# Performance work log

Hardware: AMD Instinct MI355X
Metric: run time of the kernel (lower is better)

Reference implementation:

```python
import jax, jax.numpy as jnp
import numpy as np

B, N, C, D, UP, KNN, MULT, PH = 4, 2048, 256, 64, 4, 20, 4, 64
EPS = 1e-5


def conv1d(x, w, b):
    # x: (B, Cin, N), w: (Cout, Cin)
    return jnp.einsum('oc,bcn->bon', w, x) + b[None, :, None]


def conv2d(x, w, b):
    # x: (B, Cin, N, K), 1x1 conv
    return jnp.einsum('oc,bcnk->bonk', w, x) + b[None, :, None, None]


def bn2d(x, g, bt, rm, rv):
    # eval-mode BatchNorm2d with running stats
    inv = jax.lax.rsqrt(rv + EPS)
    return g[None, :, None, None] * (x - rm[None, :, None, None]) * inv[None, :, None, None] + bt[None, :, None, None]


def group(f, idx):
    # f: (B, C, N), idx: (B, N, K) -> (B, C, N, K)
    return jax.vmap(lambda fb, ib: fb[:, ib])(f, idx)


def setup_inputs() -> dict:
    k0 = jax.random.key(0)
    ks = iter(jax.random.split(k0, 48))
    nx = lambda: next(ks)
    rn = lambda shape, s=0.05: jax.random.normal(nx(), shape, dtype=jnp.float32) * s
    z = lambda n: jnp.zeros((n,), jnp.float32)
    o = lambda n: jnp.ones((n,), jnp.float32)
    inp = {
        'pos': jax.random.normal(nx(), (B, 3, N), dtype=jnp.float32),
        'key': jax.random.normal(nx(), (B, C, N), dtype=jnp.float32),
        'query': jax.random.normal(nx(), (B, C, N), dtype=jnp.float32),
        # MLP_Res (mlp_v): in_dim=2C, hidden=C, out=C
        'wv1': rn((C, 2 * C)), 'bv1': z(C),
        'wv2': rn((C, C)), 'bv2': z(C),
        'wvs': rn((C, 2 * C)), 'bvs': z(C),
        # key/query/value projections to dim D
        'wk': rn((D, C)), 'bk': z(D),
        'wq': rn((D, C)), 'bq': z(D),
        'wval': rn((D, C)), 'bval': z(D),
        # pos_mlp: Conv2d(3,PH) -> BN -> ReLU -> Conv2d(PH,D)
        'pw1': rn((PH, 3)), 'pb1': z(PH), 'pg': o(PH), 'pbt': z(PH), 'prm': z(PH), 'prv': o(PH),
        'pw2': rn((D, PH)), 'pb2': z(D),
        # attn_mlp: Conv2d(D, D*MULT) -> BN -> ReLU -> ConvTranspose2d(D*MULT, D, (UP,1), (UP,1))
        'aw1': rn((D * MULT, D)), 'ab1': z(D * MULT), 'ag': o(D * MULT), 'abt': z(D * MULT), 'arm': z(D * MULT), 'arv': o(D * MULT),
        'ctw': rn((D * MULT, D, UP)), 'ctb': z(D),
        # conv_end: Conv1d(D, C)
        'we': rn((C, D)), 'be': z(C),
    }
    return inp


def reference(pos, key, query, wv1, bv1, wv2, bv2, wvs, bvs, wk, bk, wq, bq, wval, bval,
              pw1, pb1, pg, pbt, prm, prv, pw2, pb2,
              aw1, ab1, ag, abt, arm, arv, ctw, ctb, we, be):
    # mlp_v (MLP_Res) on concat([key, query])
    x = jnp.concatenate([key, query], axis=1)  # (B, 2C, N)
    value = conv1d(jax.nn.relu(conv1d(x, wv1, bv1)), wv2, bv2) + conv1d(x, wvs, bvs)  # (B, C, N)
    identity = value

    k_f = conv1d(key, wk, bk)      # (B, D, N)
    q_f = conv1d(query, wq, bq)    # (B, D, N)
    v_f = conv1d(value, wval, bval)

    # KNN (include_self=True): smallest-KNN indices of pairwise sq distance
    p = jnp.transpose(pos, (0, 2, 1))  # (B, N, 3)
    sq = jnp.sum(p * p, axis=-1)
    dist = sq[:, :, None] + sq[:, None, :] - 2.0 * jnp.einsum('bnc,bmc->bnm', p, p)
    idx = jax.lax.top_k(-dist, KNN)[1]  # (B, N, KNN)

    k_g = group(k_f, idx)                              # (B, D, N, KNN)
    qk_rel = q_f[:, :, :, None] - k_g
    pos_rel = pos[:, :, :, None] - group(pos, idx)     # (B, 3, N, KNN)

    h = jax.nn.relu(bn2d(conv2d(pos_rel, pw1, pb1), pg, pbt, prm, prv))
    pos_emb = conv2d(h, pw2, pb2)                      # (B, D, N, KNN)

    a = jax.nn.relu(bn2d(conv2d(qk_rel + pos_emb, aw1, ab1), ag, abt, arm, arv))  # (B, D*MULT, N, KNN)
    # ConvTranspose2d with kernel=(UP,1), stride=(UP,1): non-overlapping, out[b,o,n*UP+r,k]
    ct = jnp.einsum('bcnk,cor->bornk', a, ctw)         # (B, D, UP, N, KNN)
    Bv = a.shape[0]
    ct = jnp.transpose(ct, (0, 1, 3, 2, 4)).reshape(Bv, D, N * UP, KNN) + ctb[None, :, None, None]
    attn = jax.nn.softmax(ct, axis=-1)                 # softmax over neighbors

    v_g = group(v_f, idx) + pos_emb                    # (B, D, N, KNN)
    v_up = jnp.repeat(v_g, UP, axis=2)                 # nearest Upsample (UP,1)
    agg = jnp.sum(attn * v_up, axis=-1)                # (B, D, N*UP)
    y = conv1d(agg, we, be)                            # (B, C, N*UP)
    return y + jnp.repeat(identity, UP, axis=2)
```

## Files before the change

### kernel.cpp

```cpp
#include <hip/hip_runtime.h>
#include <hip/hip_bf16.h>

#define Bq 4
#define Nq 2048
#define Cq 256
#define Dq 64
#define UPq 4
#define KNNq 20
#define PHq 64
#define DMq 256
#define PTS 16

typedef __attribute__((ext_vector_type(8))) short short8;
typedef __attribute__((ext_vector_type(4))) short short4v;
typedef __attribute__((ext_vector_type(4))) float f32x4;
typedef __hip_bfloat16 bf16;

__device__ __forceinline__ unsigned short f2b(float x){
  bf16 h = __float2bfloat16(x);
  return *reinterpret_cast<unsigned short*>(&h);
}
__device__ __forceinline__ float b2f(short s){
  return __bfloat162float(*reinterpret_cast<bf16*>(&s));
}

__device__ __forceinline__ void swz(const float* __restrict__ src,
                                    short* __restrict__ dst,
                                    int M, int K, int g, bool transp)
{
  int j = g & 7, lane = (g >> 3) & 63, rest = g >> 9;
  int KS = K >> 5;
  int ks = rest % KS, mt = rest / KS;
  int m = mt*16 + (lane & 15);
  int k = ks*32 + ((lane >> 4) << 3) + j;
  float v = transp ? src[k*M + m] : src[m*K + k];
  dst[g] = (short)f2b(v);
}

__device__ __forceinline__ void swz_s(const float* __restrict__ src,
                                      short* __restrict__ dst,
                                      int M, int K, int g,
                                      const float* __restrict__ gam,
                                      const float* __restrict__ var)
{
  int j = g & 7, lane = (g >> 3) & 63, rest = g >> 9;
  int KS = K >> 5;
  int ks = rest % KS, mt = rest / KS;
  int m = mt*16 + (lane & 15);
  int k = ks*32 + ((lane >> 4) << 3) + j;
  float sc = gam[m] * rsqrtf(var[m] + 1e-5f);
  dst[g] = (short)f2b(src[m*K + k] * sc);
}

__global__ __launch_bounds__(256) void k_prep(
    const float* __restrict__ aw1, const float* __restrict__ ctw,
    const float* __restrict__ wv1, const float* __restrict__ wvs,
    const float* __restrict__ wv2, const float* __restrict__ wk,
    const float* __restrict__ wq,  const float* __restrict__ wval,
    const float* __restrict__ pw2, const float* __restrict__ we,
    short* __restrict__ aw1b, short* __restrict__ ctwT,
    short* __restrict__ wv1b, short* __restrict__ wvsb,
    short* __restrict__ wv2b, short* __restrict__ wkb,
    short* __restrict__ wqb,  short* __restrict__ wvalb,
    short* __restrict__ pw2b, short* __restrict__ web,
    const float* __restrict__ ag, const float* __restrict__ arv)
{
  const int t = threadIdx.x, bidx = blockIdx.x;
  if (bidx < 512){
    swz(wv1, wv1b, 256, 512, bidx*256 + t, false);
  } else if (bidx < 1024){
    swz(wvs, wvsb, 256, 512, (bidx-512)*256 + t, false);
  } else if (bidx < 1280){
    swz(wv2, wv2b, 256, 256, (bidx-1024)*256 + t, false);
  } else if (bidx < 1344){
    swz(wk, wkb, 64, 256, (bidx-1280)*256 + t, false);
  } else if (bidx < 1408){
    swz(wq, wqb, 64, 256, (bidx-1344)*256 + t, false);
  } else if (bidx < 1472){
    swz(wval, wvalb, 64, 256, (bidx-1408)*256 + t, false);
  } else if (bidx < 1488){
    swz(pw2, pw2b, 64, 64, (bidx-1472)*256 + t, false);
  } else if (bidx < 1552){
    swz_s(aw1, aw1b, 256, 64, (bidx-1488)*256 + t, ag, arv);
  } else if (bidx < 1616){
    swz(we, web, 256, 64, (bidx-1552)*256 + t, false);
  } else {
    swz(ctw, ctwT, 256, 256, (bidx-1616)*256 + t, true);
  }
}

__global__ __launch_bounds__(256, 4) void k_vk(
    const float* __restrict__ key, const float* __restrict__ query,
    const short* __restrict__ wv1b, const short* __restrict__ wvsb,
    const short* __restrict__ wv2b, const short* __restrict__ wkb,
    const short* __restrict__ wqb,  const short* __restrict__ wvalb,
    const float* __restrict__ bv1, const float* __restrict__ bv2,
    const float* __restrict__ bvs, const float* __restrict__ bk,
    const float* __restrict__ bq,  const float* __restrict__ bval,
    float* __restrict__ valueT, short* __restrict__ kfT,
    short* __restrict__ qfT,    short* __restrict__ vfT,
    const float* __restrict__ pos, int* __restrict__ idxT)
{
  const int t = threadIdx.x;
  const int lane = t & 63, w = t >> 6;
  const int vb = blockIdx.x / 5, rem = blockIdx.x % 5;

  if (rem == 4){
    __shared__ __align__(16) short Xb[16*520];
    __shared__ __align__(16) short hidB[16*264];
    __shared__ __align__(16) short valB[16*264];
    const int b = vb >> 7;
    const int n0 = (vb & 127) * PTS;
    const int quad = lane >> 4, l15 = lane & 15;

    {
      const int c4 = t >> 2, pq = t & 3;
      #pragma unroll
      for (int pass=0; pass<4; pass++){
        int c = pass*64 + c4;
        float4 kv = *reinterpret_cast<const float4*>(key   + ((size_t)(b*Cq+c))*Nq + n0 + pq*4);
        float4 qv = *reinterpret_cast<const float4*>(query + ((size_t)(b*Cq+c))*Nq + n0 + pq*4);
        const float* kf_ = (const float*)&kv;
        const float* qf_ = (const float*)&qv;
        #pragma unroll
        for (int i=0;i<4;i++){
          Xb[(pq*4+i)*520 + c]       = (short)f2b(kf_[i]);
          Xb[(pq*4+i)*520 + 256 + c] = (short)f2b(qf_[i]);
        }
      }
    }
    __syncthreads();

    f32x4 acc1[4], accS[4];
    #pragma unroll
    for (int jm=0;jm<4;jm++){ acc1[jm]=(f32x4)0.f; accS[jm]=(f32x4)0.f; }

    #pragma unroll
    for (int ks=0;ks<16;ks++){
      const int kcol = ks*32 + quad*8;
      short8 xb = *reinterpret_cast<const short8*>(&Xb[l15*520 + kcol]);
      #pragma unroll
      for (int jm=0;jm<4;jm++){
        int mt = w*4 + jm;
        short8 a1 = *reinterpret_cast<const short8*>(wv1b + ((mt*16+ks)*64 + lane)*8);
        short8 as = *reinterpret_cast<const short8*>(wvsb + ((mt*16+ks)*64 + lane)*8);
        acc1[jm] = __builtin_amdgcn_mfma_f32_16x16x32_bf16(a1, xb, acc1[jm], 0,0,0);
        accS[jm] = __builtin_amdgcn_mfma_f32_16x16x32_bf16(as, xb, accS[jm], 0,0,0);
      }
    }
    #pragma unroll
    for (int jm=0;jm<4;jm++){
      #pragma unroll
      for (int r=0;r<4;r++){
        int h = (w*4+jm)*16 + quad*4 + r;
        hidB[l15*264 + h] = (short)f2b(fmaxf(acc1[jm][r] + bv1[h], 0.f));
      }
    }
    __syncthreads();

    #pragma unroll
    for (int ks=0;ks<8;ks++){
      const int kcol = ks*32 + quad*8;
      short8 hb = *reinterpret_cast<const short8*>(&hidB[l15*264 + kcol]);
      #pragma unroll
      for (int jm=0;jm<4;jm++){
        int mt = w*4 + jm;
        short8 a = *reinterpret_cast<const short8*>(wv2b + ((mt*8+ks)*64 + lane)*8);
        accS[jm] = __builtin_amdgcn_mfma_f32_16x16x32_bf16(a, hb, accS[jm], 0,0,0);
      }
    }
    #pragma unroll
    for (int jm=0;jm<4;jm++){
      const int cb = (w*4+jm)*16 + quad*4;
      float4 v4;
      #pragma unroll
      for (int r=0;r<4;r++){
        int c = cb + r;
        float v = accS[jm][r] + bv2[c] + bvs[c];
        ((float*)&v4)[r] = v;
        valB[l15*264 + c] = (short)f2b(v);
      }
      *reinterpret_cast<float4*>(valueT + ((size_t)(b*Nq + n0 + l15))*Cq + cb) = v4;
    }
    __syncthreads();

    {
      f32x4 pk4=(f32x4)0.f, pq4=(f32x4)0.f, pv4=(f32x4)0.f;
      #pragma unroll
      for (int ks=0;ks<8;ks++){
        const int kcol = ks*32 + quad*8;
        short8 xk = *reinterpret_cast<const short8*>(&Xb[l15*520 + kcol]);
        short8 xq = *reinterpret_cast<const short8*>(&Xb[l15*520 + 256 + kcol]);
        short8 xv = *reinterpret_cast<const short8*>(&valB[l15*264 + kcol]);
        short8 ak = *reinterpret_cast<const short8*>(wkb  + ((w*8+ks)*64 + lane)*8);
        short8 aq = *reinterpret_cast<const short8*>(wqb  + ((w*8+ks)*64 + lane)*8);
        short8 av = *reinterpret_cast<const short8*>(wvalb+ ((w*8+ks)*64 + lane)*8);
        pk4 = __builtin_amdgcn_mfma_f32_16x16x32_bf16(ak, xk, pk4, 0,0,0);
        pq4 = __builtin_amdgcn_mfma_f32_16x16x32_bf16(aq, xq, pq4, 0,0,0);
        pv4 = __builtin_amdgcn_mfma_f32_16x16x32_bf16(av, xv, pv4, 0,0,0);
      }
      short4v ok, oq, ov;
      #pragma unroll
      for (int r=0;r<4;r++){
        int o = w*16 + quad*4 + r;
        ok[r] = (short)f2b(pk4[r] + bk[o]);
        oq[r] = (short)f2b(pq4[r] + bq[o]);
        ov[r] = (short)f2b(pv4[r] + bval[o]);
      }
      int n = n0 + l15;
      size_t base = ((size_t)(b*Nq+n))*Dq + w*16 + quad*4;
      *reinterpret_cast<short4v*>(kfT + base) = ok;
      *reinterpret_cast<short4v*>(qfT + base) = oq;
      *reinterpret_cast<short4v*>(vfT + base) = ov;
    }
  } else {
    const int kb = vb*4 + rem;
    const int pid = kb*4 + w;
    const int b = pid >> 11;
    const int n = pid & (Nq-1);
    const float* px = pos + (size_t)(b*3+0)*Nq;
    const float* py = pos + (size_t)(b*3+1)*Nq;
    const float* pz = pos + (size_t)(b*3+2)*Nq;
    const float xn=px[n], yn=py[n], zn=pz[n];
    const float sqn = __fadd_rn(__fadd_rn(__fmul_rn(xn,xn),__fmul_rn(yn,yn)),__fmul_rn(zn,zn));

    double kd[32];
    #pragma unroll
    for (int i=0;i<32;i++){
      int j = i*64 + lane;
      float x=px[j], y=py[j], z=pz[j];
      float sqj = __fadd_rn(__fadd_rn(__fmul_rn(x,x),__fmul_rn(y,y)),__fmul_rn(z,z));
      float dot = __fadd_rn(__fadd_rn(__fmul_rn(xn,x),__fmul_rn(yn,y)),__fmul_rn(zn,z));
      float d   = __fsub_rn(__fadd_rn(sqn,sqj), __fmul_rn(2.0f,dot));
      unsigned u = __float_as_uint(d);
      u ^= ((unsigned)((int)u >> 31)) | 0x80000000u;
      kd[i] = (double)u * 2048.0 + (double)j;
    }

    const double BIG = 9.0e15;
    double b0=BIG, b1=BIG, b2=BIG, b3=BIG;
    #pragma unroll
    for (int i=0;i<32;i++){
      double x = kd[i];
      double M0 = fmax(b0, x);  b0 = fmin(b0, x);
      double M1 = fmax(b1, M0); b1 = fmin(b1, M0);
      double M2 = fmax(b2, M1); b2 = fmin(b2, M1);
      b3 = fmin(b3, M2);
    }

    double lane_last = -1.0;
    int cnt = 0;
    for (int s=0;s<KNNq;s++){
      double m = b0;
      #pragma unroll
      for (int off=1; off<64; off<<=1)
        m = fmin(m, __shfl_xor(m, off));
      if (lane == 0){
        unsigned long long kk = (unsigned long long)m;
        idxT[(size_t)pid*KNNq + s] = (int)(kk & 2047ull);
      }
      if (b0 == m){
        lane_last = b0;
        b0 = b1; b1 = b2; b2 = b3; b3 = BIG;
        cnt++;
      }
      if (__any(cnt >= 4)){
        if (cnt >= 4){
          b0 = BIG; b1 = BIG; b2 = BIG; b3 = BIG;
          #pragma unroll
          for (int i=0;i<32;i++){
            double x = (kd[i] > lane_last) ? kd[i] : BIG;
            double M0 = fmax(b0, x);  b0 = fmin(b0, x);
            double M1 = fmax(b1, M0); b1 = fmin(b1, M0);
            double M2 = fmax(b2, M1); b2 = fmin(b2, M1);
            b3 = fmin(b3, M2);
          }
          cnt = 0;
        }
      }
    }
  }
}

#define UADDR(row, colb) ((((row)*128 + (colb)) ^ (((row)&7)<<4)))
#define SADDR(row, colb) ((((row)*256 + (colb)) ^ (((row)&7)<<4)))

__global__ __launch_bounds__(256, 4) void k_attn(
  const float* __restrict__ pos,
  const float* __restrict__ valueT, const short* __restrict__ kfT,
  const short* __restrict__ qfT,    const short* __restrict__ vfT,
  const int* __restrict__ idxT,
  const float* __restrict__ pw1, const float* __restrict__ pb1,
  const float* __restrict__ pg,  const float* __restrict__ pbt,
  const float* __restrict__ prm, const float* __restrict__ prv,
  const short* __restrict__ pw2b, const float* __restrict__ pb2,
  const short* __restrict__ aw1b, const float* __restrict__ ab1,
  const float* __restrict__ ag,  const float* __restrict__ abt,
  const float* __restrict__ arm, const float* __restrict__ arv,
  const short* __restrict__ ctwT,
  const short* __restrict__ web,  const float* __restrict__ be,
  float* __restrict__ out)
{
  __shared__ __align__(16) char unionA[22528];
  __shared__ __align__(16) char unionB[6144];
  __shared__ __align__(16) char unionC[6144];
  __shared__ __align__(16) short vgB[64*42];

  float* sh2S = (float*)(unionA + 12288);
  float* prl  = (float*)unionC;
  int*   nb   = (int*)(unionC + 576);

  const int t = threadIdx.x;
  const int b  = blockIdx.x >> 10;
  const int n0 = (blockIdx.x & 1023) * 2;
  const int lane = t & 63, quad = lane >> 4, l15 = lane & 15, w = t >> 6;
  const size_t bN = (size_t)b * Nq;
  const int obase = w*16 + quad*4;

  if (t < 48){
    int p = (t >= 24);
    int k = t - p*24;
    int nn = n0 + p;
    int j = (k < KNNq) ? idxT[(bN + nn)*KNNq + k] : nn;
    nb[t] = j;
    #pragma unroll
    for (int d=0; d<3; d++){
      prl[d*48+t] = pos[((size_t)(b*3+d))*Nq + nn] - pos[((size_t)(b*3+d))*Nq + j];
    }
  }
  {
    float sc = ag[t] * rsqrtf(arv[t] + 1e-5f);
    sh2S[t]  = ab1[t]*sc + (abt[t] - arm[t]*sc);
  }
  __syncthreads();

  short4v pq4[3], pk4[3], pv4[3];
  #pragma unroll
  for (int nt=0; nt<3; nt++){
    int pk = nt*16 + l15;
    int p  = (pk >= 24);
    int j  = nb[pk];
    pq4[nt] = *reinterpret_cast<const short4v*>(qfT + (bN + n0 + p)*Dq + obase);
    pk4[nt] = *reinterpret_cast<const short4v*>(kfT + (bN + j)*Dq + obase);
    pv4[nt] = *reinterpret_cast<const short4v*>(vfT + (bN + j)*Dq + obase);
  }

  {
    const int ph = t & 63;
    float sc = pg[ph] * rsqrtf(prv[ph] + 1e-5f);
    float w0 = pw1[ph*3+0]*sc, w1 = pw1[ph*3+1]*sc, w2 = pw1[ph*3+2]*sc;
    float bb = pb1[ph]*sc + (pbt[ph] - prm[ph]*sc);
    #pragma unroll
    for (int m=0;m<12;m++){
      int pk = w + m*4;
      float h = fmaf(w0, prl[pk], fmaf(w1, prl[48+pk], fmaf(w2, prl[96+pk], bb)));
      *(short*)(unionB + UADDR(pk, ph*2)) = (short)f2b(fmaxf(h, 0.f));
    }
  }
  __syncthreads();

  {
    f32x4 accP[3];
    #pragma unroll
    for (int nt=0;nt<3;nt++) accP[nt]=(f32x4)0.f;
    #pragma unroll
    for (int ks=0;ks<2;ks++){
      const int kcolb = (ks*32 + quad*8)*2;
      short8 a = *reinterpret_cast<const short8*>(pw2b + ((w*2+ks)*64 + lane)*8);
      #pragma unroll
      for (int nt=0;nt<3;nt++){
        short8 bb = *reinterpret_cast<const short8*>(unionB + UADDR(nt*16+l15, kcolb));
        accP[nt] = __builtin_amdgcn_mfma_f32_16x16x32_bf16(a, bb, accP[nt], 0,0,0);
      }
    }
    #pragma unroll
    for (int nt=0;nt<3;nt++){
      int pk = nt*16 + l15;
      bool vld = (pk < 20) || (pk >= 24 && pk < 44);
      int col  = pk - (pk >= 24 ? 4 : 0);
      short4v ut4;
      #pragma unroll
      for (int r=0;r<4;r++){
        int o = obase + r;
        float pe = accP[nt][r] + pb2[o];
        ut4[r] = (short)f2b((b2f(pq4[nt][r]) - b2f(pk4[nt][r])) + pe);
        if (vld) vgB[o*42 + col] = (short)f2b(b2f(pv4[nt][r]) + pe);
      }
      *(short4v*)(unionC + UADDR(pk, obase*2)) = ut4;
    }
  }
  __syncthreads();

  f32x4 accT[4][3];
  #pragma unroll
  for (int jm=0;jm<4;jm++)
    #pragma unroll
    for (int nt=0;nt<3;nt++) accT[jm][nt]=(f32x4)0.f;

  #pragma unroll
  for (int ch=0; ch<2; ch++){
    f32x4 accC[2][3];
    #pragma unroll
    for (int jm=0;jm<2;jm++)
      #pragma unroll
      for (int nt=0;nt<3;nt++) accC[jm][nt]=(f32x4)0.f;
    __builtin_amdgcn_s_setprio(1);
    #pragma unroll
    for (int ks=0;ks<2;ks++){
      const int kcolb = (ks*32 + quad*8)*2;
      short8 bb[3];
      #pragma unroll
      for (int nt=0;nt<3;nt++)
        bb[nt] = *reinterpret_cast<const short8*>(unionC + UADDR(nt*16+l15, kcolb));
      #pragma unroll
      for (int jm=0;jm<2;jm++){
        int mt = ch*8 + w*2 + jm;
        short8 a = *reinterpret_cast<const short8*>(aw1b + ((mt*2+ks)*64 + lane)*8);
        #pragma unroll
        for (int nt=0;nt<3;nt++)
          accC[jm][nt] = __builtin_amdgcn_mfma_f32_16x16x32_bf16(a, bb[nt], accC[jm][nt], 0,0,0);
      }
    }
    __builtin_amdgcn_s_setprio(0);

    short8 actw0[4];
    #pragma unroll
    for (int jm=0;jm<4;jm++)
      actw0[jm] = *reinterpret_cast<const short8*>(ctwT + (((w*4+jm)*8 + ch*4)*64 + lane)*8);

    if (ch == 1) __syncthreads();
    #pragma unroll
    for (int jm=0;jm<2;jm++){
      const int colb = ((w*2+jm)*16 + quad*4)*2;
      #pragma unroll
      for (int nt=0;nt<3;nt++){
        int pk = nt*16 + l15;
        short4v pkv;
        #pragma unroll
        for (int r=0;r<4;r++){
          int c = ch*128 + (w*2+jm)*16 + quad*4 + r;
          pkv[r] = (short)f2b(fmaxf(accC[jm][nt][r] + sh2S[c], 0.f));
        }
        *(short4v*)(unionA + SADDR(pk, colb)) = pkv;
      }
    }
    __syncthreads();
    __builtin_amdgcn_s_setprio(1);
    #pragma unroll
    for (int ksl=0; ksl<4; ksl++){
      const int kcolb = (ksl*32 + quad*8)*2;
      short8 bb[3];
      #pragma unroll
      for (int nt=0;nt<3;nt++)
        bb[nt] = *reinterpret_cast<const short8*>(unionA + SADDR(nt*16+l15, kcolb));
      #pragma unroll
      for (int jm=0;jm<4;jm++){
        int mt = w*4 + jm;
        short8 a = (ksl == 0) ? actw0[jm]
                 : *reinterpret_cast<const short8*>(ctwT + ((mt*8 + ch*4 + ksl)*64 + lane)*8);
        #pragma unroll
        for (int nt=0;nt<3;nt++)
          accT[jm][nt] = __builtin_amdgcn_mfma_f32_16x16x32_bf16(a, bb[nt], accT[jm][nt], 0,0,0);
      }
    }
    __builtin_amdgcn_s_setprio(0);
  }
  __syncthreads();

  #pragma unroll
  for (int nt=0;nt<3;nt++){
    int pk = nt*16 + l15;
    bool vld = (pk < 20) || (pk >= 24 && pk < 44);
    int col  = pk - (pk >= 24 ? 4 : 0);
    if (vld){
      #pragma unroll
      for (int jm=0;jm<4;jm++){
        #pragma unroll
        for (int r=0;r<4;r++){
          int row = (w*4+jm)*16 + quad*4 + r;
          *(short*)(unionA + row*88 + col*2) = (short)f2b(accT[jm][nt][r]);
        }
      }
    }
  }
  __syncthreads();

  float4 idv[4];
  if (l15 < 8){
    int p = l15 >> 2;
    #pragma unroll
    for (int jm=0;jm<4;jm++)
      idv[jm] = *reinterpret_cast<const float4*>(valueT + (bN + n0 + p)*Cq + (w*4+jm)*16 + quad*4);
  }
  short8 aweb[2][4];
  #pragma unroll
  for (int ks=0;ks<2;ks++)
    #pragma unroll
    for (int jm=0;jm<4;jm++)
      aweb[ks][jm] = *reinterpret_cast<const short8*>(web + (((w*4+jm)*2+ks)*64 + lane)*8);
  {
    const int o = t >> 2, rr = t & 3;
    #pragma unroll
    for (int p=0;p<2;p++){
      float ct[20];
      #pragma unroll
      for (int q=0;q<5;q++){
        short4v cv = *reinterpret_cast<const short4v*>(unionA + t*88 + p*40 + q*8);
        #pragma unroll
        for (int i=0;i<4;i++) ct[q*4+i] = b2f(cv[i]);
      }
      float m = ct[0];
      #pragma unroll
      for (int k=1;k<20;k++) m = fmaxf(m, ct[k]);
      float s = 0.f, a = 0.f;
      #pragma unroll
      for (int q=0;q<5;q++){
        short4v vv = *reinterpret_cast<const short4v*>((const char*)vgB + o*84 + p*40 + q*8);
        #pragma unroll
        for (int i=0;i<4;i++){
          float e = __expf(ct[q*4+i] - m);
          s += e;
          a = fmaf(e, b2f(vv[i]), a);
        }
      }
      *(short*)(unionB + UADDR(p*4+rr, o*2)) = (short)f2b(__fdividef(a, s));
    }
  }
  __syncthreads();

  {
    f32x4 accE[4];
    #pragma unroll
    for (int jm=0;jm<4;jm++) accE[jm]=(f32x4)0.f;
    __builtin_amdgcn_s_setprio(1);
    #pragma unroll
    for (int ks=0;ks<2;ks++){
      const int kcolb = (ks*32 + quad*8)*2;
      short8 bb = *reinterpret_cast<const short8*>(unionB + UADDR(l15, kcolb));
      #pragma unroll
      for (int jm=0;jm<4;jm++){
        accE[jm] = __builtin_amdgcn_mfma_f32_16x16x32_bf16(aweb[ks][jm], bb, accE[jm], 0,0,0);
      }
    }
    __builtin_amdgcn_s_setprio(0);
    if (l15 < 8){
      int p = l15 >> 2, rr = l15 & 3;
      #pragma unroll
      for (int jm=0;jm<4;jm++){
        float4 b4 = *reinterpret_cast<const float4*>(be + (w*4+jm)*16 + quad*4);
        #pragma unroll
        for (int r=0;r<4;r++){
          int c = (w*4+jm)*16 + quad*4 + r;
          float y = accE[jm][r] + ((const float*)&b4)[r] + ((const float*)&idv[jm])[r];
          out[((size_t)(b*Cq+c))*((size_t)Nq*UPq) + (size_t)(n0+p)*UPq + rr] = y;
        }
      }
    }
  }
}

extern "C" void kernel_launch(void* const* d_in, const int* in_sizes, int n_in,
                              void* d_out, int out_size, void* d_ws, size_t ws_size,
                              hipStream_t stream)
{
  const float* pos  = (const float*)d_in[0];
  const float* key  = (const float*)d_in[1];
  const float* qry  = (const float*)d_in[2];
  const float* wv1  = (const float*)d_in[3];
  const float* bv1  = (const float*)d_in[4];
  const float* wv2  = (const float*)d_in[5];
  const float* bv2  = (const float*)d_in[6];
  const float* wvs  = (const float*)d_in[7];
  const float* bvs  = (const float*)d_in[8];
  const float* wk   = (const float*)d_in[9];
  const float* bk   = (const float*)d_in[10];
  const float* wq   = (const float*)d_in[11];
  const float* bq   = (const float*)d_in[12];
  const float* wval = (const float*)d_in[13];
  const float* bval = (const float*)d_in[14];
  const float* pw1  = (const float*)d_in[15];
  const float* pb1  = (const float*)d_in[16];
  const float* pg   = (const float*)d_in[17];
  const float* pbt  = (const float*)d_in[18];
  const float* prm  = (const float*)d_in[19];
  const float* prv  = (const float*)d_in[20];
  const float* pw2  = (const float*)d_in[21];
  const float* pb2  = (const float*)d_in[22];
  const float* aw1  = (const float*)d_in[23];
  const float* ab1  = (const float*)d_in[24];
  const float* ag   = (const float*)d_in[25];
  const float* abt  = (const float*)d_in[26];
  const float* arm  = (const float*)d_in[27];
  const float* arv  = (const float*)d_in[28];
  const float* ctw  = (const float*)d_in[29];
  const float* we   = (const float*)d_in[31];
  const float* be   = (const float*)d_in[32];

  char* ws = (char*)d_ws;
  float* valueT = (float*)(ws);
  short* kfT    = (short*)(ws + 8388608);
  short* qfT    = (short*)(ws + 9437184);
  short* vfT    = (short*)(ws + 10485760);
  int*   idxT   = (int*)  (ws + 11534336);
  short* aw1b   = (short*)(ws + 12189696);
  short* ctwT   = (short*)(ws + 12222464);
  short* wv1b   = (short*)(ws + 12353536);
  short* wvsb   = (short*)(ws + 12615680);
  short* wv2b   = (short*)(ws + 12877824);
  short* wkb    = (short*)(ws + 13008896);
  short* wqb    = (short*)(ws + 13041664);
  short* wvalb  = (short*)(ws + 13074432);
  short* pw2b   = (short*)(ws + 13107200);
  short* web    = (short*)(ws + 13115392);
  float* out    = (float*)d_out;

  k_prep<<<dim3(1872), dim3(256), 0, stream>>>(
      aw1, ctw, wv1, wvs, wv2, wk, wq, wval, pw2, we,
      aw1b, ctwT, wv1b, wvsb, wv2b, wkb, wqb, wvalb, pw2b, web,
      ag, arv);
  k_vk<<<dim3(2560), dim3(256), 0, stream>>>(
      key, qry, wv1b, wvsb, wv2b, wkb, wqb, wvalb,
      bv1, bv2, bvs, bk, bq, bval,
      valueT, kfT, qfT, vfT, pos, idxT);
  k_attn<<<dim3(Bq*Nq/2), dim3(256), 0, stream>>>(
      pos, valueT, kfT, qfT, vfT, idxT,
      pw1, pb1, pg, pbt, prm, prv, pw2b, pb2,
      aw1b, ab1, ag, abt, arm, arv, ctwT, web, be, out);
}
```

Measured before the change: 247.2 us.

## Compute softmax-aggregation directly from MFMA accumulators via cross-lane shuffles

Swaps the MFMA operand order so the transposed-conv accumulators hold neighbors along rows, then performs the softmax max, exp, sum and weighted aggregation in registers using wave shuffles. This removes the bf16 round-trip of the logits through shared memory and two block barriers, and shrinks the shared buffer, which may raise occupancy. In exchange it adds shuffle reductions and some redundant exp work on padded lanes, and it keeps the logits in fp32 instead of rounding them to bf16.

```diff
diff --git a/kernel.cpp b/kernel.cpp
--- a/kernel.cpp
+++ b/kernel.cpp
@@ -301,7 +301,7 @@
   const short* __restrict__ web,  const float* __restrict__ be,
   float* __restrict__ out)
 {
-  __shared__ __align__(16) char unionA[22528];
+  __shared__ __align__(16) char unionA[13312];
   __shared__ __align__(16) char unionB[6144];
   __shared__ __align__(16) char unionC[6144];
   __shared__ __align__(16) short vgB[64*42];
@@ -460,30 +460,11 @@
                  : *reinterpret_cast<const short8*>(ctwT + ((mt*8 + ch*4 + ksl)*64 + lane)*8);
         #pragma unroll
         for (int nt=0;nt<3;nt++)
-          accT[jm][nt] = __builtin_amdgcn_mfma_f32_16x16x32_bf16(a, bb[nt], accT[jm][nt], 0,0,0);
+          accT[jm][nt] = __builtin_amdgcn_mfma_f32_16x16x32_bf16(bb[nt], a, accT[jm][nt], 0,0,0);
       }
     }
     __builtin_amdgcn_s_setprio(0);
   }
-  __syncthreads();
-
-  #pragma unroll
-  for (int nt=0;nt<3;nt++){
-    int pk = nt*16 + l15;
-    bool vld = (pk < 20) || (pk >= 24 && pk < 44);
-    int col  = pk - (pk >= 24 ? 4 : 0);
-    if (vld){
-      #pragma unroll
-      for (int jm=0;jm<4;jm++){
-        #pragma unroll
-        for (int r=0;r<4;r++){
-          int row = (w*4+jm)*16 + quad*4 + r;
-          *(short*)(unionA + row*88 + col*2) = (short)f2b(accT[jm][nt][r]);
-        }
-      }
-    }
-  }
-  __syncthreads();
 
   float4 idv[4];
   if (l15 < 8){
@@ -498,32 +479,58 @@
     #pragma unroll
     for (int jm=0;jm<4;jm++)
       aweb[ks][jm] = *reinterpret_cast<const short8*>(web + (((w*4+jm)*2+ks)*64 + lane)*8);
+
   {
-    const int o = t >> 2, rr = t & 3;
-    #pragma unroll
-    for (int p=0;p<2;p++){
-      float ct[20];
-      #pragma unroll
-      for (int q=0;q<5;q++){
-        short4v cv = *reinterpret_cast<const short4v*>(unionA + t*88 + p*40 + q*8);
-        #pragma unroll
-        for (int i=0;i<4;i++) ct[q*4+i] = b2f(cv[i]);
-      }
-      float m = ct[0];
-      #pragma unroll
-      for (int k=1;k<20;k++) m = fmaxf(m, ct[k]);
-      float s = 0.f, a = 0.f;
-      #pragma unroll
-      for (int q=0;q<5;q++){
-        short4v vv = *reinterpret_cast<const short4v*>((const char*)vgB + o*84 + p*40 + q*8);
-        #pragma unroll
-        for (int i=0;i<4;i++){
-          float e = __expf(ct[q*4+i] - m);
-          s += e;
-          a = fmaf(e, b2f(vv[i]), a);
-        }
-      }
-      *(short*)(unionB + UADDR(p*4+rr, o*2)) = (short)f2b(__fdividef(a, s));
+    #pragma unroll
+    for (int jm=0;jm<4;jm++){
+      float m0 = -1e30f, m1 = -1e30f;
+      #pragma unroll
+      for (int r=0;r<4;r++) m0 = fmaxf(m0, accT[jm][0][r]);
+      float g1 = fmaxf(fmaxf(accT[jm][1][0],accT[jm][1][1]),
+                       fmaxf(accT[jm][1][2],accT[jm][1][3]));
+      float g2 = fmaxf(fmaxf(accT[jm][2][0],accT[jm][2][1]),
+                       fmaxf(accT[jm][2][2],accT[jm][2][3]));
+      if (quad == 0) m0 = fmaxf(m0, g1);
+      if (quad >= 2) m1 = fmaxf(m1, g1);
+      if (quad <= 2) m1 = fmaxf(m1, g2);
+      m0 = fmaxf(m0, __shfl_xor(m0, 16)); m0 = fmaxf(m0, __shfl_xor(m0, 32));
+      m1 = fmaxf(m1, __shfl_xor(m1, 16)); m1 = fmaxf(m1, __shfl_xor(m1, 32));
+
+      const int o = (w*4+jm)*4 + (l15 >> 2);
+      float s0 = 0.f, s1 = 0.f, pv0 = 0.f, pv1 = 0.f;
+      #pragma unroll
+      for (int r=0;r<4;r++){
+        float e = __expf(accT[jm][0][r] - m0);
+        s0 += e;
+        pv0 = fmaf(e, b2f(vgB[o*42 + quad*4 + r]), pv0);
+      }
+      #pragma unroll
+      for (int r=0;r<4;r++){
+        bool isp0 = (quad == 0), vld = (quad != 1);
+        float mm = isp0 ? m0 : m1;
+        float e  = vld ? __expf(accT[jm][1][r] - mm) : 0.f;
+        int col  = isp0 ? (16 + r) : (vld ? (12 + quad*4 + r) : 0);
+        float vg = b2f(vgB[o*42 + col]);
+        if (isp0){ s0 += e; pv0 = fmaf(e, vg, pv0); }
+        else     { s1 += e; pv1 = fmaf(e, vg, pv1); }
+      }
+      #pragma unroll
+      for (int r=0;r<4;r++){
+        bool vld = (quad <= 2);
+        float e = vld ? __expf(accT[jm][2][r] - m1) : 0.f;
+        int col = vld ? (28 + quad*4 + r) : 0;
+        s1 += e;
+        pv1 = fmaf(e, b2f(vgB[o*42 + col]), pv1);
+      }
+      s0  += __shfl_xor(s0, 16);  s0  += __shfl_xor(s0, 32);
+      s1  += __shfl_xor(s1, 16);  s1  += __shfl_xor(s1, 32);
+      pv0 += __shfl_xor(pv0, 16); pv0 += __shfl_xor(pv0, 32);
+      pv1 += __shfl_xor(pv1, 16); pv1 += __shfl_xor(pv1, 32);
+      if (quad == 0){
+        int rr = l15 & 3;
+        *(short*)(unionB + UADDR(rr,     o*2)) = (short)f2b(__fdividef(pv0, s0));
+        *(short*)(unionB + UADDR(4 + rr, o*2)) = (short)f2b(__fdividef(pv1, s1));
+      }
     }
   }
   __syncthreads();
```

After: 260.2 us. +5.3%, slower.
